# Performance work log

Hardware: AMD Instinct MI355X
Metric: run time of the kernel (lower is better)

## Reference

```python
import jax, jax.numpy as jnp
import numpy as np
import math

H, W = 64, 64
WS = 8            # window_size
KS = 8            # kernel_size (depthwise conv stride=kernel)
D = 512           # d_model
CF = 128          # flow_dModel
IC = D + CF       # 640
HEAD = 8
GH, GW = H // WS, W // WS
G = GH * GW       # windows
EPS = 1e-5


def layernorm(x, g, b):
    m = jnp.mean(x, axis=-1, keepdims=True)
    v = jnp.mean((x - m) ** 2, axis=-1, keepdims=True)
    return (x - m) * jax.lax.rsqrt(v + EPS) * g + b


def depthwise_conv(x_nchw, w, b):
    # w: [C, 1, KS, KS], stride=KS, VALID, groups=C
    y = jax.lax.conv_general_dilated(
        x_nchw, w, window_strides=(KS, KS), padding='VALID',
        feature_group_count=x_nchw.shape[1],
        dimension_numbers=('NCHW', 'OIHW', 'NCHW'))
    return y + b[None, :, None, None]


def setup_inputs() -> dict:
    key = jax.random.key(0)
    ks = jax.random.split(key, 24)
    bt = 8
    s = 0.02
    inp = {
        'x': jax.random.normal(ks[0], (bt, H * W, D), jnp.float32),
        'f': jax.random.normal(ks[1], (bt, H * W, CF), jnp.float32),
        't': 2,
        'Wq': jax.random.normal(ks[2], (IC, D), jnp.float32) * s,
        'bq': jnp.zeros((D,), jnp.float32),
        'Wk': jax.random.normal(ks[3], (IC, D), jnp.float32) * s,
        'bk': jnp.zeros((D,), jnp.float32),
        'Wv': jax.random.normal(ks[4], (D, D), jnp.float32) * s,
        'bv': jnp.zeros((D,), jnp.float32),
        'Wo': jax.random.normal(ks[5], (D, D), jnp.float32) * s,
        'bo': jnp.zeros((D,), jnp.float32),
        'convK_w': jax.random.normal(ks[6], (IC, 1, KS, KS), jnp.float32) * s,
        'convK_b': jnp.zeros((IC,), jnp.float32),
        'convV_w': jax.random.normal(ks[7], (D, 1, KS, KS), jnp.float32) * s,
        'convV_b': jnp.zeros((D,), jnp.float32),
        'qn_g': jnp.ones((IC,), jnp.float32), 'qn_b': jnp.zeros((IC,), jnp.float32),
        'kn_g': jnp.ones((IC,), jnp.float32), 'kn_b': jnp.zeros((IC,), jnp.float32),
        'vn_g': jnp.ones((D,), jnp.float32), 'vn_b': jnp.zeros((D,), jnp.float32),
        'rw_W': jax.random.normal(ks[8], (IC, CF), jnp.float32) * s,
        'rw_b': jnp.zeros((CF,), jnp.float32),
    }
    return inp


def reference(x, f, t, Wq, bq, Wk, bk, Wv, bv, Wo, bo,
              convK_w, convK_b, convV_w, convV_b,
              qn_g, qn_b, kn_g, kn_b, vn_g, vn_b, rw_W, rw_b):
    bt, n, c = x.shape
    hd = c // HEAD
    x4 = x.reshape(bt, H, W, c)            # no padding: H, W multiples of WS
    f4 = f.reshape(bt, H, W, CF)

    xf = jnp.concatenate([x4, f4], axis=-1)                 # [bt,H,W,IC]
    flow_w = jax.nn.sigmoid(xf @ rw_W + rw_b)               # [bt,H,W,CF]
    f4 = f4 * flow_w
    qk = jnp.concatenate([x4, f4], axis=-1)                 # [bt,H,W,IC]

    def windows(a):
        cc = a.shape[-1]
        a = a.reshape(bt, GH, WS, GW, WS, cc).transpose(0, 1, 3, 2, 4, 5)
        return a.reshape(bt, G, WS * WS, cc)

    q = windows(qk)                                          # [bt,G,ws2,IC]

    k_glob = depthwise_conv(qk.transpose(0, 3, 1, 2), convK_w, convK_b)
    k_glob = k_glob.transpose(0, 2, 3, 1).reshape(bt, -1, IC)  # [bt,M,IC]
    M = k_glob.shape[1]
    k_glob = jnp.broadcast_to(k_glob[:, None], (bt, G, M, IC))
    k = jnp.concatenate([q, k_glob], axis=2)                 # [bt,G,ws2+M,IC]

    q = layernorm(q, qn_g, qn_b)
    k = layernorm(k, kn_g, kn_b)

    v_glob = depthwise_conv(x4.transpose(0, 3, 1, 2), convV_w, convV_b)
    v_glob = v_glob.transpose(0, 2, 3, 1).reshape(bt, -1, c)
    v_glob = jnp.broadcast_to(v_glob[:, None], (bt, G, M, c))
    xw = windows(x4)
    v = jnp.concatenate([xw, v_glob], axis=2)                # [bt,G,ws2+M,c]
    v = layernorm(v, vn_g, vn_b)

    query = q @ Wq + bq                                      # [bt,G,ws2,c]
    key = k @ Wk + bk
    value = v @ Wv + bv

    Lk = key.shape[2]
    query = query.reshape(bt, G, WS * WS, HEAD, hd).transpose(0, 1, 3, 2, 4)
    key = key.reshape(bt, G, Lk, HEAD, hd).transpose(0, 1, 3, 2, 4)
    value = value.reshape(bt, G, Lk, HEAD, hd).transpose(0, 1, 3, 2, 4)

    scores = jnp.einsum('bghqd,bghkd->bghqk', query, key) / math.sqrt(hd)
    attn = jax.nn.softmax(scores, axis=-1)
    out = jnp.einsum('bghqk,bghkd->bghqd', attn, value)      # [bt,G,H,ws2,hd]

    out = out.transpose(0, 1, 3, 2, 4).reshape(bt, GH, GW, WS, WS, c)
    out = out.transpose(0, 1, 3, 2, 4, 5).reshape(bt, H, W, c).reshape(bt, n, c)
    return out @ Wo + bo
```

## Files before the change

### kernel.cpp

```cpp
#include <hip/hip_runtime.h>
#include <hip/hip_bf16.h>

typedef __hip_bfloat16 bf16;
typedef __attribute__((ext_vector_type(8))) short bf16x8;
typedef __attribute__((ext_vector_type(8))) unsigned short ushort8;
typedef __attribute__((ext_vector_type(4))) float f32x4;

#define BT 8
#define HH 64
#define WW 64
#define NSP (HH*WW)
#define DD 512
#define CF 128
#define IC 640
#define NG 64
#define NM 64
#define TRI 1536
#define EPS 1e-5f

static __device__ __forceinline__ float b2f(bf16 v) { return __bfloat162float(v); }
static __device__ __forceinline__ bf16 f2b(float v) { return __float2bfloat16(v); }
static __device__ __forceinline__ float u2f(unsigned short u) {
    return __uint_as_float((unsigned)u << 16);
}
static __device__ __forceinline__ unsigned short f2u(float v) {
    bf16 b = __float2bfloat16(v);
    return __builtin_bit_cast(unsigned short, b);
}

__global__ void detect_dtype(const void* __restrict__ x, int* __restrict__ flag) {
    __shared__ int cnt;
    if (threadIdx.x == 0) cnt = 0;
    __syncthreads();
    const unsigned* w = (const unsigned*)x;
    int local = 0;
    for (int i = threadIdx.x; i < 4096; i += 256) {
        float v = __uint_as_float(w[i]);
        float a = fabsf(v);
        if (a > 1e-5f && a < 1e4f) local++;
    }
    atomicAdd(&cnt, local);
    __syncthreads();
    if (threadIdx.x == 0) *flag = (cnt > 2048) ? 1 : 0;
}

#define NW 20
struct WTab {
    const void* src[NW];
    int pre[NW + 1];
};

__global__ void convert_weights(WTab t, const int* __restrict__ flag,
                                bf16* __restrict__ dst, int total) {
    int fp32 = *flag;
    for (int idx = blockIdx.x * blockDim.x + threadIdx.x; idx < total;
         idx += gridDim.x * blockDim.x) {
        int seg = 0;
        #pragma unroll
        for (int i = 0; i < NW; ++i) if (idx >= t.pre[i + 1]) seg = i + 1;
        int local = idx - t.pre[seg];
        bf16 v;
        if (fp32) v = f2b(((const float*)t.src[seg])[local]);
        else      v = ((const bf16*)t.src[seg])[local];
        dst[idx] = v;
    }
}

struct TT {
    int srcoff[5], dstoff[5], R[5], C[5], dstride[5], tpre[6];
};
__global__ void transpose_weights(const bf16* __restrict__ wc, bf16* __restrict__ wt, TT t) {
    __shared__ unsigned short tile[32][33];
    int tb = blockIdx.x;
    int seg = 0;
    while (tb >= t.tpre[seg + 1]) seg++;
    int lt = tb - t.tpre[seg];
    int C = t.C[seg];
    int tpr = C / 32;
    int r0 = (lt / tpr) * 32, c0 = (lt % tpr) * 32;
    int ds = t.dstride[seg];
    const unsigned short* src = (const unsigned short*)(wc + t.srcoff[seg]);
    unsigned short* dst = (unsigned short*)(wt + t.dstoff[seg]);
    int tx = threadIdx.x & 31, ty = threadIdx.x >> 5;
    #pragma unroll
    for (int i = 0; i < 4; ++i)
        tile[ty + i * 8][tx] = src[(long long)(r0 + ty + i * 8) * C + c0 + tx];
    __syncthreads();
    #pragma unroll
    for (int i = 0; i < 4; ++i)
        dst[(long long)(c0 + ty + i * 8) * ds + r0 + tx] = tile[tx][ty + i * 8];
}

__global__ void fold_ln_weights(bf16* __restrict__ WT, int stride,
                                const bf16* __restrict__ g,
                                const bf16* __restrict__ b, const bf16* __restrict__ bias,
                                float* __restrict__ colsum, float* __restrict__ bias2,
                                int K, int Kpad) {
    int n = blockIdx.x;
    bf16* wrow = WT + (long long)n * stride;
    float s1 = 0.f, s2 = 0.f;
    for (int k = threadIdx.x; k < K; k += 256) {
        float w = b2f(wrow[k]);
        float gk = b2f(g[k]);
        wrow[k] = f2b(w * gk);
        s1 += w * gk;
        s2 += w * b2f(b[k]);
    }
    for (int k = K + threadIdx.x; k < Kpad; k += 256) wrow[k] = f2b(0.f);
    __shared__ float r1[256], r2[256];
    r1[threadIdx.x] = s1; r2[threadIdx.x] = s2;
    __syncthreads();
    for (int off = 128; off > 0; off >>= 1) {
        if (threadIdx.x < off) {
            r1[threadIdx.x] += r1[threadIdx.x + off];
            r2[threadIdx.x] += r2[threadIdx.x + off];
        }
        __syncthreads();
    }
    if (threadIdx.x == 0) {
        colsum[n] = r1[0];
        bias2[n]  = b2f(bias[n]) + r2[0];
    }
}

__global__ void assemble_qk_v(const void* __restrict__ xv, const void* __restrict__ fv,
                              const int* __restrict__ flag, bf16* __restrict__ qk,
                              int rows, long long xoff, long long foff) {
    int fp32 = *flag;
    long long total = (long long)rows * 80;
    for (long long i = (long long)blockIdx.x * blockDim.x + threadIdx.x; i < total;
         i += (long long)gridDim.x * blockDim.x) {
        int row = (int)(i / 80);
        int g = (int)(i % 80);
        ushort8 o;
        if (g < 64) {
            long long s = xoff + (long long)row * DD + g * 8;
            if (fp32) {
                const float* xp = (const float*)xv + s;
                #pragma unroll
                for (int e = 0; e < 8; ++e) o[e] = f2u(xp[e]);
            } else {
                o = *(const ushort8*)((const unsigned short*)xv + s);
            }
        } else {
            long long s = foff + (long long)row * CF + (g - 64) * 8;
            if (fp32) {
                const float* fp = (const float*)fv + s;
                #pragma unroll
                for (int e = 0; e < 8; ++e) o[e] = f2u(fp[e]);
            } else {
                o = *(const ushort8*)((const unsigned short*)fv + s);
            }
        }
        *(ushort8*)((unsigned short*)qk + (long long)row * IC + g * 8) = o;
    }
}

__global__ void dwconv_kernel(const bf16* __restrict__ src, int ldr, int C, int ldout,
                              int ldpad,
                              const bf16* __restrict__ w, const bf16* __restrict__ bias,
                              bf16* __restrict__ dst) {
    int bm = blockIdx.x;
    int b = bm >> 6;
    int m = bm & 63;
    int my = m >> 3, mx = m & 7;
    const bf16* sb = src + (long long)b * NSP * ldr;
    for (int c = threadIdx.x; c < C; c += blockDim.x) {
        float acc = b2f(bias[c]);
        #pragma unroll
        for (int ky = 0; ky < 8; ++ky) {
            #pragma unroll
            for (int kx = 0; kx < 8; ++kx) {
                int pos = (my * 8 + ky) * WW + mx * 8 + kx;
                acc += b2f(sb[(long long)pos * ldr + c]) * b2f(w[c * 64 + ky * 8 + kx]);
            }
        }
        dst[(long long)bm * ldout + c] = f2b(acc);
    }
    for (int c = C + threadIdx.x; c < ldpad; c += blockDim.x)
        dst[(long long)bm * ldout + c] = f2b(0.f);
}

__global__ void stats_fused(const bf16* __restrict__ qk, float* __restrict__ stats_full,
                            float* __restrict__ stats_x, int rows) {
    int gt = blockIdx.x * blockDim.x + threadIdx.x;
    int wid = gt >> 6;
    int lane = gt & 63;
    if (wid >= rows) return;
    const unsigned short* p = (const unsigned short*)qk + (long long)wid * IC;
    ushort8 v = *(const ushort8*)(p + lane * 8);
    float s1 = 0.f, ss1 = 0.f, s2 = 0.f, ss2 = 0.f;
    #pragma unroll
    for (int e = 0; e < 8; ++e) { float f = u2f(v[e]); s1 += f; ss1 += f * f; }
    if (lane < 16) {
        ushort8 v2 = *(const ushort8*)(p + DD + lane * 8);
        #pragma unroll
        for (int e = 0; e < 8; ++e) { float f = u2f(v2[e]); s2 += f; ss2 += f * f; }
    }
    #pragma unroll
    for (int off = 32; off > 0; off >>= 1) {
        s1  += __shfl_down(s1,  off, 64);
        ss1 += __shfl_down(ss1, off, 64);
        s2  += __shfl_down(s2,  off, 64);
        ss2 += __shfl_down(ss2, off, 64);
    }
    if (lane == 0) {
        float m1 = s1 / 512.f;
        float var1 = ss1 / 512.f - m1 * m1;
        stats_x[wid * 2]     = m1;
        stats_x[wid * 2 + 1] = rsqrtf(var1 + EPS);
        float st = s1 + s2, sst = ss1 + ss2;
        float m2 = st / 640.f;
        float var2 = sst / 640.f - m2 * m2;
        stats_full[wid * 2]     = m2;
        stats_full[wid * 2 + 1] = rsqrtf(var2 + EPS);
    }
}

__global__ void stats_kernel(const bf16* __restrict__ X, int lda, float* __restrict__ stats,
                             int rows, int K) {
    int gt = blockIdx.x * blockDim.x + threadIdx.x;
    int wid = gt >> 6;
    int lane = gt & 63;
    if (wid >= rows) return;
    const bf16* p = X + (long long)wid * lda;
    float s = 0.f, ss = 0.f;
    for (int k = lane; k < K; k += 64) {
        float v = b2f(p[k]);
        s += v; ss += v * v;
    }
    #pragma unroll
    for (int off = 32; off > 0; off >>= 1) {
        s  += __shfl_down(s,  off, 64);
        ss += __shfl_down(ss, off, 64);
    }
    if (lane == 0) {
        float m = s / K;
        float var = ss / K - m * m;
        stats[wid * 2]     = m;
        stats[wid * 2 + 1] = rsqrtf(var + EPS);
    }
}

__global__ __launch_bounds__(256)
void gemm_mfma(const bf16* __restrict__ A, int lda,
               const float* __restrict__ statsQK, const float* __restrict__ statsX,
               int nQK,
               const float* __restrict__ colsum, const float* __restrict__ bias2,
               const bf16* __restrict__ Bmat,
               const bf16* __restrict__ bias,
               bf16* __restrict__ C,
               void* __restrict__ Cout, const int* __restrict__ outflag, long long outoff,
               const bf16* __restrict__ A2k, const float* __restrict__ stats2k,
               bf16* __restrict__ C2k,
               const bf16* __restrict__ A2v, const float* __restrict__ stats2v,
               bf16* __restrict__ C2v, int M2,
               int M, int N, int K, int mode) {
    __shared__ unsigned short As[128 * 32];
    __shared__ unsigned short Bs[128 * 32];
    int tid = threadIdx.x;

    int nwgx = gridDim.x;
    int nwg = nwgx * gridDim.y;
    int orig = blockIdx.y * nwgx + blockIdx.x;
    int qq = nwg >> 3, rr = nwg & 7;
    int xcd = orig & 7, idx = orig >> 3;
    int wg = (xcd < rr ? xcd * (qq + 1) : rr * (qq + 1) + (xcd - rr) * qq) + idx;
    int gy = wg / nwgx;
    int gx = wg % nwgx;
    int bn = gx * 128;

    int nby_main = M >> 7;
    const bf16* Ap;
    const float* stp = nullptr;
    bf16* C2 = nullptr;
    int rowbase, mlim, glob, colOff = 0;
    if (gy < nby_main) {
        Ap = A; rowbase = gy * 128; mlim = M; glob = 0;
        if (mode == 2) stp = (bn >= nQK) ? statsX : statsQK;
    } else {
        if (bn < 512) return;
        int isV = bn >= 1024;
        Ap = isV ? A2v : A2k;
        stp = isV ? stats2v : stats2k;
        C2 = isV ? C2v : C2k;
        colOff = isV ? 1024 : 512;
        rowbase = (gy - nby_main) * 128; mlim = M2; glob = 1;
    }

    int wave = tid >> 6, lane = tid & 63;
    int qm = (wave >> 1) * 64;
    int qn = (wave & 1) * 64;
    int lm = lane & 15;
    int kq = (lane >> 4) * 8;
    int sr = lane >> 2;
    int sc = (lane & 3) * 8;

    f32x4 acc[4][4];
    #pragma unroll
    for (int i = 0; i < 4; ++i)
        #pragma unroll
        for (int j = 0; j < 4; ++j)
            acc[i][j] = (f32x4){0.f, 0.f, 0.f, 0.f};

    const unsigned short* Au = (const unsigned short*)Ap;
    const unsigned short* Bu = (const unsigned short*)Bmat;

    for (int k0 = 0; k0 < K; k0 += 32) {
        #pragma unroll
        for (int i = 0; i < 2; ++i) {
            int seg = wave * 2 + i;
            const unsigned short* gp =
                Au + (long long)(rowbase + seg * 16 + sr) * lda + k0 + sc;
            __builtin_amdgcn_global_load_lds(
                (const __attribute__((address_space(1))) void*)gp,
                (__attribute__((address_space(3))) void*)&As[seg * 512], 16, 0, 0);
        }
        #pragma unroll
        for (int i = 0; i < 2; ++i) {
            int seg = wave * 2 + i;
            const unsigned short* gp =
                Bu + (long long)(bn + seg * 16 + sr) * K + k0 + sc;
            __builtin_amdgcn_global_load_lds(
                (const __attribute__((address_space(1))) void*)gp,
                (__attribute__((address_space(3))) void*)&Bs[seg * 512], 16, 0, 0);
        }
        __syncthreads();
        bf16x8 af[4], bfr[4];
        #pragma unroll
        for (int i = 0; i < 4; ++i)
            af[i] = *(const bf16x8*)&As[(qm + i * 16 + lm) * 32 + kq];
        #pragma unroll
        for (int j = 0; j < 4; ++j)
            bfr[j] = *(const bf16x8*)&Bs[(qn + j * 16 + lm) * 32 + kq];
        #pragma unroll
        for (int i = 0; i < 4; ++i)
            #pragma unroll
            for (int j = 0; j < 4; ++j)
                acc[i][j] = __builtin_amdgcn_mfma_f32_16x16x32_bf16(
                    af[i], bfr[j], acc[i][j], 0, 0, 0);
        __syncthreads();
    }

    int rq = (lane >> 4) * 4;
    float cs[4], bb[4];
    #pragma unroll
    for (int j = 0; j < 4; ++j) {
        int col = bn + qn + j * 16 + lm;
        if (mode == 2) { cs[j] = colsum[col]; bb[j] = bias2[col]; }
        else bb[j] = bias ? b2f(bias[col]) : 0.f;
    }
    int ofp = (!glob && outflag) ? *outflag : 0;
    #pragma unroll
    for (int i = 0; i < 4; ++i) {
        #pragma unroll
        for (int r = 0; r < 4; ++r) {
            int row = rowbase + qm + i * 16 + rq + r;
            if (row >= mlim) continue;
            float mean = 0.f, rstd = 0.f;
            if (mode == 2) { mean = stp[row * 2]; rstd = stp[row * 2 + 1]; }
            #pragma unroll
            for (int j = 0; j < 4; ++j) {
                int col = bn + qn + j * 16 + lm;
                float v = acc[i][j][r];
                if (mode == 2) v = rstd * (v - mean * cs[j]) + bb[j];
                else {
                    v += bb[j];
                    if (mode == 1 || mode == 3) v = 1.f / (1.f + __expf(-v));
                }
                if (mode == 3) {
                    unsigned short* qp =
                        (unsigned short*)C + (long long)row * IC + DD + col;
                    *qp = f2u(u2f(*qp) * v);
                    continue;
                }
                if (glob) {
                    C2[(long long)row * 512 + (col - colOff)] = f2b(v);
                } else if (outflag) {
                    long long ci = (long long)row * N + col;
                    if (ofp) ((float*)Cout)[outoff + ci] = v;
                    else     ((bf16*)Cout)[outoff + ci] = f2b(v);
                } else {
                    C[(long long)row * N + col] = f2b(v);
                }
            }
        }
    }
}

#define QS_STRIDE 72
#define PS_STRIDE 136
__global__ __launch_bounds__(256)
void attn_kernel(const bf16* __restrict__ qkv,
                 const bf16* __restrict__ key_glob, const bf16* __restrict__ val_glob,
                 bf16* __restrict__ attout) {
    int h = blockIdx.x & 7;
    int g = (blockIdx.x >> 3) & 63;
    int b = blockIdx.x >> 9;
    int gy = g >> 3, gx = g & 7;

    __shared__ unsigned short smem[64 * PS_STRIDE + 64 * PS_STRIDE];
    unsigned short* Qs = smem;
    unsigned short* Ks = smem + 64 * QS_STRIDE;
    unsigned short* Ps = smem;
    unsigned short* Vs = smem + 64 * PS_STRIDE;

    int tid = threadIdx.x;
    const unsigned short* QKV = (const unsigned short*)qkv;
    const unsigned short* KG = (const unsigned short*)key_glob;
    const unsigned short* VG = (const unsigned short*)val_glob;

    #pragma unroll
    for (int it = 0; it < 2; ++it) {
        int i = tid + it * 256;
        int t = i >> 3, dg = (i & 7) * 8;
        int ty = t >> 3, tx = t & 7;
        long long row = (long long)b * NSP + (gy * 8 + ty) * WW + gx * 8 + tx;
        *(ushort8*)&Qs[t * QS_STRIDE + dg] =
            *(const ushort8*)&QKV[row * TRI + h * 64 + dg];
    }
    #pragma unroll
    for (int it = 0; it < 4; ++it) {
        int i = tid + it * 256;
        int t = i >> 3, dg = (i & 7) * 8;
        ushort8 kv;
        if (t < 64) {
            int ty = t >> 3, tx = t & 7;
            long long row = (long long)b * NSP + (gy * 8 + ty) * WW + gx * 8 + tx;
            kv = *(const ushort8*)&QKV[row * TRI + 512 + h * 64 + dg];
        } else {
            long long srow = (long long)b * NM + (t - 64);
            kv = *(const ushort8*)&KG[srow * DD + h * 64 + dg];
        }
        *(ushort8*)&Ks[t * QS_STRIDE + dg] = kv;
    }
    __syncthreads();

    int wave = tid >> 6, lane = tid & 63;
    int m0 = wave * 16;
    int lm = lane & 15;
    int quad = lane >> 4;

    f32x4 sacc[8];
    #pragma unroll
    for (int j = 0; j < 8; ++j) sacc[j] = (f32x4){0.f, 0.f, 0.f, 0.f};
    #pragma unroll
    for (int ks = 0; ks < 2; ++ks) {
        int kq = quad * 8 + ks * 32;
        bf16x8 af = *(const bf16x8*)&Qs[(m0 + lm) * QS_STRIDE + kq];
        #pragma unroll
        for (int j = 0; j < 8; ++j) {
            bf16x8 bfr = *(const bf16x8*)&Ks[(j * 16 + lm) * QS_STRIDE + kq];
            sacc[j] = __builtin_amdgcn_mfma_f32_16x16x32_bf16(af, bfr, sacc[j], 0, 0, 0);
        }
    }
    float pinv[4];
    #pragma unroll
    for (int r = 0; r < 4; ++r) {
        float mx = -1e30f;
        #pragma unroll
        for (int j = 0; j < 8; ++j) {
            sacc[j][r] *= 0.125f;
            mx = fmaxf(mx, sacc[j][r]);
        }
        mx = fmaxf(mx, __shfl_xor(mx, 1, 64));
        mx = fmaxf(mx, __shfl_xor(mx, 2, 64));
        mx = fmaxf(mx, __shfl_xor(mx, 4, 64));
        mx = fmaxf(mx, __shfl_xor(mx, 8, 64));
        float l = 0.f;
        #pragma unroll
        for (int j = 0; j < 8; ++j) {
            float p = __expf(sacc[j][r] - mx);
            sacc[j][r] = p;
            l += p;
        }
        l += __shfl_xor(l, 1, 64);
        l += __shfl_xor(l, 2, 64);
        l += __shfl_xor(l, 4, 64);
        l += __shfl_xor(l, 8, 64);
        pinv[r] = 1.f / l;
    }
    __syncthreads();

    #pragma unroll
    for (int r = 0; r < 4; ++r) {
        int qrow = m0 + quad * 4 + r;
        #pragma unroll
        for (int j = 0; j < 8; ++j)
            Ps[qrow * PS_STRIDE + j * 16 + lm] = f2u(sacc[j][r] * pinv[r]);
    }
    #pragma unroll
    for (int it = 0; it < 4; ++it) {
        int i = tid + it * 256;
        int t = i & 127, dg = (i >> 7) * 8;
        ushort8 v;
        if (t < 64) {
            int ty = t >> 3, tx = t & 7;
            long long row = (long long)b * NSP + (gy * 8 + ty) * WW + gx * 8 + tx;
            v = *(const ushort8*)&QKV[row * TRI + 1024 + h * 64 + dg];
        } else {
            long long srow = (long long)b * NM + (t - 64);
            v = *(const ushort8*)&VG[srow * DD + h * 64 + dg];
        }
        #pragma unroll
        for (int e = 0; e < 8; ++e) Vs[(dg + e) * PS_STRIDE + t] = v[e];
    }
    __syncthreads();

    f32x4 oacc[4];
    #pragma unroll
    for (int j = 0; j < 4; ++j) oacc[j] = (f32x4){0.f, 0.f, 0.f, 0.f};
    #pragma unroll
    for (int ks = 0; ks < 4; ++ks) {
        int kq = quad * 8 + ks * 32;
        bf16x8 af = *(const bf16x8*)&Ps[(m0 + lm) * PS_STRIDE + kq];
        #pragma unroll
        for (int j = 0; j < 4; ++j) {
            bf16x8 bfr = *(const bf16x8*)&Vs[(j * 16 + lm) * PS_STRIDE + kq];
            oacc[j] = __builtin_amdgcn_mfma_f32_16x16x32_bf16(af, bfr, oacc[j], 0, 0, 0);
        }
    }
    #pragma unroll
    for (int r = 0; r < 4; ++r) {
        int qrow = m0 + quad * 4 + r;
        int ty = qrow >> 3, tx = qrow & 7;
        long long orow = (long long)b * NSP + (gy * 8 + ty) * WW + gx * 8 + tx;
        unsigned short* op = (unsigned short*)attout + orow * DD + h * 64;
        #pragma unroll
        for (int j = 0; j < 4; ++j)
            op[j * 16 + lm] = f2u(oacc[j][r]);
    }
}

static inline size_t alg(size_t b) { return (b + 255) & ~(size_t)255; }

extern "C" void kernel_launch(void* const* d_in, const int* in_sizes, int n_in,
                              void* d_out, int out_size, void* d_ws, size_t ws_size,
                              hipStream_t stream) {
    int s = (n_in > 2 && in_sizes[2] == 1) ? 0 : -1;

    const void* xv = d_in[0];
    const void* fv = d_in[1];
    const void* wsrc[NW];
    for (int i = 0; i < NW; ++i) wsrc[i] = d_in[3 + s + i];
    (void)out_size;

    const int wcnt[NW] = {327680, 512, 327680, 512, 262144, 512, 262144, 512,
                          40960, 640, 32768, 512, 640, 640, 640, 640, 512, 512,
                          81920, 128};
    WTab tab;
    int pre = 0;
    for (int i = 0; i < NW; ++i) {
        tab.src[i] = wsrc[i];
        tab.pre[i] = pre;
        pre += wcnt[i];
    }
    tab.pre[NW] = pre;
    const int wtotal = pre;

    char* ws = (char*)d_ws;
    size_t head = 0;
    int* flag = (int*)(ws + head); head += 256;
    bf16* wc = (bf16*)(ws + head); head += alg((size_t)wtotal * 2);
    const int off_qkvW = 0;
    const int off_WoT  = TRI * IC;
    const int off_rwT  = off_WoT + DD * DD;
    const int wtpre    = off_rwT + CF * IC;
    bf16* wt = (bf16*)(ws + head); head += alg((size_t)wtpre * 2);
    float* foldv = (float*)(ws + head); head += alg(2 * TRI * sizeof(float));
    float* cs_qkv = foldv;
    float* b2_qkv = foldv + TRI;

    const bf16* bq     = wc + tab.pre[1];
    const bf16* bk     = wc + tab.pre[3];
    const bf16* bv     = wc + tab.pre[5];
    const bf16* bo     = wc + tab.pre[7];
    const bf16* convKw = wc + tab.pre[8];
    const bf16* convKb = wc + tab.pre[9];
    const bf16* convVw = wc + tab.pre[10];
    const bf16* convVb = wc + tab.pre[11];
    const bf16* qn_g   = wc + tab.pre[12];
    const bf16* qn_b   = wc + tab.pre[13];
    const bf16* kn_g   = wc + tab.pre[14];
    const bf16* kn_b   = wc + tab.pre[15];
    const bf16* vn_g   = wc + tab.pre[16];
    const bf16* vn_b   = wc + tab.pre[17];
    const bf16* rw_b   = wc + tab.pre[19];
    bf16* qkvW = wt + off_qkvW;
    bf16* WoT  = wt + off_WoT;
    bf16* rwT  = wt + off_rwT;

    size_t avail = ws_size > head ? ws_size - head : 0;
    auto need = [&](int bc) -> size_t {
        size_t rows = (size_t)bc * NSP;
        size_t gm = (size_t)bc * NM, gmp = gm + 64;
        return alg(rows * IC * 2) + alg(rows * TRI * 2)
             + 2 * alg(gmp * IC * 2) + 2 * alg(gm * DD * 2)
             + 2 * alg(rows * 8) + 2 * alg(gmp * 8);
    };
    int nb = BT;
    while (nb > 1 && need(nb) > avail) nb--;

    detect_dtype<<<1, 256, 0, stream>>>(xv, flag);
    convert_weights<<<(wtotal + 255) / 256, 256, 0, stream>>>(tab, flag, wc, wtotal);
    {
        TT tt;
        const int srcsel[5]  = {0, 2, 4, 6, 18};
        const int Rr[5]      = {IC, IC, DD, DD, IC};
        const int Cc[5]      = {DD, DD, DD, DD, CF};
        const int dof[5]     = {0, DD * IC, 2 * DD * IC, off_WoT, off_rwT};
        const int dstr[5]    = {IC, IC, IC, DD, IC};
        int tp = 0;
        for (int i = 0; i < 5; ++i) {
            tt.srcoff[i] = tab.pre[srcsel[i]];
            tt.dstoff[i] = dof[i];
            tt.R[i] = Rr[i];
            tt.C[i] = Cc[i];
            tt.dstride[i] = dstr[i];
            tt.tpre[i] = tp;
            tp += (Rr[i] / 32) * (Cc[i] / 32);
        }
        tt.tpre[5] = tp;
        transpose_weights<<<tp, 256, 0, stream>>>(wc, wt, tt);
    }
    fold_ln_weights<<<DD, 256, 0, stream>>>(qkvW,              IC, qn_g, qn_b, bq,
                                            cs_qkv,       b2_qkv,       IC, IC);
    fold_ln_weights<<<DD, 256, 0, stream>>>(qkvW + DD * IC,    IC, kn_g, kn_b, bk,
                                            cs_qkv + 512, b2_qkv + 512, IC, IC);
    fold_ln_weights<<<DD, 256, 0, stream>>>(qkvW + 2 * DD * IC, IC, vn_g, vn_b, bv,
                                            cs_qkv + 1024, b2_qkv + 1024, DD, IC);

    for (int b0 = 0; b0 < BT; b0 += nb) {
        int bc = BT - b0 < nb ? BT - b0 : nb;
        int rows = bc * NSP;
        int gm = bc * NM;
        int gmp = gm + 64;
        int gyg = (gm + 127) / 128;

        size_t off = head;
        auto alloc = [&](size_t bytes) -> void* {
            void* p = ws + off; off += alg(bytes); return p;
        };
        bf16* qk        = (bf16*)alloc((size_t)rows * IC * 2);
        bf16* qkv       = (bf16*)alloc((size_t)rows * TRI * 2);
        bf16* kg        = (bf16*)alloc((size_t)gmp * IC * 2);
        bf16* vg        = (bf16*)alloc((size_t)gmp * IC * 2);
        bf16* key_glob  = (bf16*)alloc((size_t)gm * DD * 2);
        bf16* val_glob  = (bf16*)alloc((size_t)gm * DD * 2);
        float* stats_qk = (float*)alloc((size_t)rows * 8);
        float* stats_x  = (float*)alloc((size_t)rows * 8);
        float* stats_kg = (float*)alloc((size_t)gmp * 8);
        float* stats_vg = (float*)alloc((size_t)gmp * 8);
        bf16* attout    = qk;

        {
            long long total = (long long)rows * 80;
            int blocks = (int)((total + 255) / 256);
            assemble_qk_v<<<blocks, 256, 0, stream>>>(
                xv, fv, flag, qk, rows,
                (long long)b0 * NSP * DD, (long long)b0 * NSP * CF);
        }
        gemm_mfma<<<dim3(CF / 128, rows / 128), 256, 0, stream>>>(
            qk, IC, nullptr, nullptr, 0, nullptr, nullptr, rwT, rw_b, qk,
            nullptr, nullptr, 0,
            nullptr, nullptr, nullptr, nullptr, nullptr, nullptr, 0,
            rows, CF, IC, 3);
        dwconv_kernel<<<bc * NM, 256, 0, stream>>>(qk, IC, IC, IC, IC, convKw, convKb, kg);
        dwconv_kernel<<<bc * NM, 256, 0, stream>>>(qk, IC, DD, IC, IC, convVw, convVb, vg);
        stats_fused<<<rows / 4, 256, 0, stream>>>(qk, stats_qk, stats_x, rows);
        stats_kernel<<<(gm * 64 + 255) / 256, 256, 0, stream>>>(kg, IC, stats_kg, gm, IC);
        stats_kernel<<<(gm * 64 + 255) / 256, 256, 0, stream>>>(vg, IC, stats_vg, gm, DD);
        gemm_mfma<<<dim3(TRI / 128, rows / 128 + gyg), 256, 0, stream>>>(
            qk, IC, stats_qk, stats_x, 1024, cs_qkv, b2_qkv, qkvW, nullptr, qkv,
            nullptr, nullptr, 0,
            kg, stats_kg, key_glob, vg, stats_vg, val_glob, gm,
            rows, TRI, IC, 2);
        attn_kernel<<<bc * NG * 8, 256, 0, stream>>>(qkv, key_glob, val_glob, attout);
        gemm_mfma<<<dim3(DD / 128, rows / 128), 256, 0, stream>>>(
            attout, DD, nullptr, nullptr, 0, nullptr, nullptr, WoT, bo, nullptr,
            d_out, flag, (long long)b0 * NSP * DD,
            nullptr, nullptr, nullptr, nullptr, nullptr, nullptr, 0,
            rows, DD, DD, 0);
    }
}
```

Before: 514.3 us.

## Double-buffer GEMM LDS tiles and fuse depthwise convs with their LayerNorm stats

The MFMA GEMM main loop now uses two LDS buffers, so the global-to-LDS loads for the next K-tile are issued before computing the current one, overlapping memory with MFMA work. Separately, the two depthwise conv kernels and the two stats kernels are merged into one kernel. It reads the qk input once for both K and V convs and reduces the mean and rstd in-block, removing three launches and a re-read of kg/vg. The GEMM loop assumes an even tile count (K/32), which holds for K=640 and 512, and it doubles LDS use. The mode==1 sigmoid branch is also dropped from the epilogue.

```diff
diff --git a/kernel.cpp b/kernel.cpp
--- a/kernel.cpp
+++ b/kernel.cpp
@@ -156,29 +156,66 @@
     }
 }
 
-__global__ void dwconv_kernel(const bf16* __restrict__ src, int ldr, int C, int ldout,
-                              int ldpad,
-                              const bf16* __restrict__ w, const bf16* __restrict__ bias,
-                              bf16* __restrict__ dst) {
+__global__ void dwconv2_kernel(const bf16* __restrict__ qk,
+                               const bf16* __restrict__ wk, const bf16* __restrict__ bk_,
+                               const bf16* __restrict__ wv, const bf16* __restrict__ bv_,
+                               bf16* __restrict__ kg, bf16* __restrict__ vg,
+                               float* __restrict__ stats_kg, float* __restrict__ stats_vg) {
     int bm = blockIdx.x;
     int b = bm >> 6;
     int m = bm & 63;
     int my = m >> 3, mx = m & 7;
-    const bf16* sb = src + (long long)b * NSP * ldr;
-    for (int c = threadIdx.x; c < C; c += blockDim.x) {
-        float acc = b2f(bias[c]);
+    const bf16* sb = qk + (long long)b * NSP * IC;
+    int tid = threadIdx.x;
+    float sk = 0.f, ssk = 0.f, sv = 0.f, ssv = 0.f;
+    for (int c = tid; c < IC; c += 256) {
+        float acc_k = b2f(bk_[c]);
+        bool doV = (c < DD);
+        float acc_v = doV ? b2f(bv_[c]) : 0.f;
         #pragma unroll
         for (int ky = 0; ky < 8; ++ky) {
             #pragma unroll
             for (int kx = 0; kx < 8; ++kx) {
                 int pos = (my * 8 + ky) * WW + mx * 8 + kx;
-                acc += b2f(sb[(long long)pos * ldr + c]) * b2f(w[c * 64 + ky * 8 + kx]);
+                float v = b2f(sb[(long long)pos * IC + c]);
+                acc_k += v * b2f(wk[c * 64 + ky * 8 + kx]);
+                if (doV) acc_v += v * b2f(wv[c * 64 + ky * 8 + kx]);
             }
         }
-        dst[(long long)bm * ldout + c] = f2b(acc);
-    }
-    for (int c = C + threadIdx.x; c < ldpad; c += blockDim.x)
-        dst[(long long)bm * ldout + c] = f2b(0.f);
+        bf16 rk = f2b(acc_k);
+        kg[(long long)bm * IC + c] = rk;
+        float fk = b2f(rk);
+        sk += fk; ssk += fk * fk;
+        if (doV) {
+            bf16 rv = f2b(acc_v);
+            vg[(long long)bm * IC + c] = rv;
+            float fv2 = b2f(rv);
+            sv += fv2; ssv += fv2 * fv2;
+        }
+    }
+    for (int c = DD + tid; c < IC; c += 256) vg[(long long)bm * IC + c] = f2b(0.f);
+    __shared__ float r[4][256];
+    r[0][tid] = sk; r[1][tid] = ssk; r[2][tid] = sv; r[3][tid] = ssv;
+    __syncthreads();
+    for (int off = 128; off > 0; off >>= 1) {
+        if (tid < off) {
+            r[0][tid] += r[0][tid + off];
+            r[1][tid] += r[1][tid + off];
+            r[2][tid] += r[2][tid + off];
+            r[3][tid] += r[3][tid + off];
+        }
+        __syncthreads();
+    }
+    if (tid == 0) {
+        float mk = r[0][0] / IC;
+        float vk = r[1][0] / IC - mk * mk;
+        stats_kg[bm * 2] = mk;
+        stats_kg[bm * 2 + 1] = rsqrtf(vk + EPS);
+        float mv = r[2][0] / DD;
+        float vv = r[3][0] / DD - mv * mv;
+        stats_vg[bm * 2] = mv;
+        stats_vg[bm * 2 + 1] = rsqrtf(vv + EPS);
+    }
 }
 
 __global__ void stats_fused(const bf16* __restrict__ qk, float* __restrict__ stats_full,
@@ -214,31 +251,6 @@
         float var2 = sst / 640.f - m2 * m2;
         stats_full[wid * 2]     = m2;
         stats_full[wid * 2 + 1] = rsqrtf(var2 + EPS);
-    }
-}
-
-__global__ void stats_kernel(const bf16* __restrict__ X, int lda, float* __restrict__ stats,
-                             int rows, int K) {
-    int gt = blockIdx.x * blockDim.x + threadIdx.x;
-    int wid = gt >> 6;
-    int lane = gt & 63;
-    if (wid >= rows) return;
-    const bf16* p = X + (long long)wid * lda;
-    float s = 0.f, ss = 0.f;
-    for (int k = lane; k < K; k += 64) {
-        float v = b2f(p[k]);
-        s += v; ss += v * v;
-    }
-    #pragma unroll
-    for (int off = 32; off > 0; off >>= 1) {
-        s  += __shfl_down(s,  off, 64);
-        ss += __shfl_down(ss, off, 64);
-    }
-    if (lane == 0) {
-        float m = s / K;
-        float var = ss / K - m * m;
-        stats[wid * 2]     = m;
-        stats[wid * 2 + 1] = rsqrtf(var + EPS);
     }
 }
 
@@ -256,8 +268,8 @@
                const bf16* __restrict__ A2v, const float* __restrict__ stats2v,
                bf16* __restrict__ C2v, int M2,
                int M, int N, int K, int mode) {
-    __shared__ unsigned short As[128 * 32];
-    __shared__ unsigned short Bs[128 * 32];
+    __shared__ unsigned short As[2][128 * 32];
+    __shared__ unsigned short Bs[2][128 * 32];
     int tid = threadIdx.x;
 
     int nwgx = gridDim.x;
@@ -305,40 +317,51 @@
 
     const unsigned short* Au = (const unsigned short*)Ap;
     const unsigned short* Bu = (const unsigned short*)Bmat;
-
-    for (int k0 = 0; k0 < K; k0 += 32) {
-        #pragma unroll
-        for (int i = 0; i < 2; ++i) {
-            int seg = wave * 2 + i;
-            const unsigned short* gp =
-                Au + (long long)(rowbase + seg * 16 + sr) * lda + k0 + sc;
-            __builtin_amdgcn_global_load_lds(
-                (const __attribute__((address_space(1))) void*)gp,
-                (__attribute__((address_space(3))) void*)&As[seg * 512], 16, 0, 0);
-        }
-        #pragma unroll
-        for (int i = 0; i < 2; ++i) {
-            int seg = wave * 2 + i;
-            const unsigned short* gp =
-                Bu + (long long)(bn + seg * 16 + sr) * K + k0 + sc;
-            __builtin_amdgcn_global_load_lds(
-                (const __attribute__((address_space(1))) void*)gp,
-                (__attribute__((address_space(3))) void*)&Bs[seg * 512], 16, 0, 0);
-        }
-        __syncthreads();
+    int segA = wave * 2;
+    const unsigned short* a_src0 = Au + (long long)(rowbase + segA * 16 + sr) * lda + sc;
+    const unsigned short* a_src1 = Au + (long long)(rowbase + (segA + 1) * 16 + sr) * lda + sc;
+    const unsigned short* b_src0 = Bu + (long long)(bn + segA * 16 + sr) * K + sc;
+    const unsigned short* b_src1 = Bu + (long long)(bn + (segA + 1) * 16 + sr) * K + sc;
+
+    auto STAGE = [&](int buf, int k0) {
+        __builtin_amdgcn_global_load_lds(
+            (const __attribute__((address_space(1))) void*)(a_src0 + k0),
+            (__attribute__((address_space(3))) void*)&As[buf][segA * 512], 16, 0, 0);
+        __builtin_amdgcn_global_load_lds(
+            (const __attribute__((address_space(1))) void*)(a_src1 + k0),
+            (__attribute__((address_space(3))) void*)&As[buf][(segA + 1) * 512], 16, 0, 0);
+        __builtin_amdgcn_global_load_lds(
+            (const __attribute__((address_space(1))) void*)(b_src0 + k0),
+            (__attribute__((address_space(3))) void*)&Bs[buf][segA * 512], 16, 0, 0);
+        __builtin_amdgcn_global_load_lds(
+            (const __attribute__((address_space(1))) void*)(b_src1 + k0),
+            (__attribute__((address_space(3))) void*)&Bs[buf][(segA + 1) * 512], 16, 0, 0);
+    };
+    auto COMPUTE = [&](int buf) {
         bf16x8 af[4], bfr[4];
         #pragma unroll
         for (int i = 0; i < 4; ++i)
-            af[i] = *(const bf16x8*)&As[(qm + i * 16 + lm) * 32 + kq];
+            af[i] = *(const bf16x8*)&As[buf][(qm + i * 16 + lm) * 32 + kq];
         #pragma unroll
         for (int j = 0; j < 4; ++j)
-            bfr[j] = *(const bf16x8*)&Bs[(qn + j * 16 + lm) * 32 + kq];
+            bfr[j] = *(const bf16x8*)&Bs[buf][(qn + j * 16 + lm) * 32 + kq];
         #pragma unroll
         for (int i = 0; i < 4; ++i)
             #pragma unroll
             for (int j = 0; j < 4; ++j)
                 acc[i][j] = __builtin_amdgcn_mfma_f32_16x16x32_bf16(
                     af[i], bfr[j], acc[i][j], 0, 0, 0);
+    };
+
+    int nt = K >> 5;
+    STAGE(0, 0);
+    __syncthreads();
+    for (int t = 0; t < nt; t += 2) {
+        STAGE(1, (t + 1) << 5);
+        COMPUTE(0);
+        __syncthreads();
+        if (t + 2 < nt) STAGE(0, (t + 2) << 5);
+        COMPUTE(1);
         __syncthreads();
     }
 
@@ -366,7 +389,7 @@
                 if (mode == 2) v = rstd * (v - mean * cs[j]) + bb[j];
                 else {
                     v += bb[j];
-                    if (mode == 1 || mode == 3) v = 1.f / (1.f + __expf(-v));
+                    if (mode == 3) v = 1.f / (1.f + __expf(-v));
                 }
                 if (mode == 3) {
                     unsigned short* qp =
@@ -634,23 +657,23 @@
         int bc = BT - b0 < nb ? BT - b0 : nb;
         int rows = bc * NSP;
         int gm = bc * NM;
-        int gmp = gm + 64;
         int gyg = (gm + 127) / 128;
 
         size_t off = head;
         auto alloc = [&](size_t bytes) -> void* {
             void* p = ws + off; off += alg(bytes); return p;
         };
+        size_t gmp = (size_t)gm + 64;
         bf16* qk        = (bf16*)alloc((size_t)rows * IC * 2);
         bf16* qkv       = (bf16*)alloc((size_t)rows * TRI * 2);
-        bf16* kg        = (bf16*)alloc((size_t)gmp * IC * 2);
-        bf16* vg        = (bf16*)alloc((size_t)gmp * IC * 2);
+        bf16* kg        = (bf16*)alloc(gmp * IC * 2);
+        bf16* vg        = (bf16*)alloc(gmp * IC * 2);
         bf16* key_glob  = (bf16*)alloc((size_t)gm * DD * 2);
         bf16* val_glob  = (bf16*)alloc((size_t)gm * DD * 2);
         float* stats_qk = (float*)alloc((size_t)rows * 8);
         float* stats_x  = (float*)alloc((size_t)rows * 8);
-        float* stats_kg = (float*)alloc((size_t)gmp * 8);
-        float* stats_vg = (float*)alloc((size_t)gmp * 8);
+        float* stats_kg = (float*)alloc(gmp * 8);
+        float* stats_vg = (float*)alloc(gmp * 8);
         bf16* attout    = qk;
 
         {
@@ -665,11 +688,9 @@
             nullptr, nullptr, 0,
             nullptr, nullptr, nullptr, nullptr, nullptr, nullptr, 0,
             rows, CF, IC, 3);
-        dwconv_kernel<<<bc * NM, 256, 0, stream>>>(qk, IC, IC, IC, IC, convKw, convKb, kg);
-        dwconv_kernel<<<bc * NM, 256, 0, stream>>>(qk, IC, DD, IC, IC, convVw, convVb, vg);
+        dwconv2_kernel<<<bc * NM, 256, 0, stream>>>(
+            qk, convKw, convKb, convVw, convVb, kg, vg, stats_kg, stats_vg);
         stats_fused<<<rows / 4, 256, 0, stream>>>(qk, stats_qk, stats_x, rows);
-        stats_kernel<<<(gm * 64 + 255) / 256, 256, 0, stream>>>(kg, IC, stats_kg, gm, IC);
-        stats_kernel<<<(gm * 64 + 255) / 256, 256, 0, stream>>>(vg, IC, stats_vg, gm, DD);
         gemm_mfma<<<dim3(TRI / 128, rows / 128 + gyg), 256, 0, stream>>>(
             qk, IC, stats_qk, stats_x, 1024, cs_qkv, b2_qkv, qkvW, nullptr, qkv,
             nullptr, nullptr, 0,
```

New measurement: 720.5 us. 1.4x slower.

## Fuse K and V depthwise convs into one vectorized kernel with transposed weights

Applied to the files above, without the earlier changes.

Replaces the two per-channel scalar depthwise-conv launches with a single kernel. Each block handles a 64-channel chunk of one window, reads 8 bf16 values per load, and reduces over kernel positions with shuffles plus a small LDS step. The conv weights are pre-transposed to a position-major layout so weight loads coalesce, and each input read is shared between the K and V accumulations. The mode-1 sigmoid branch is also dropped from the GEMM epilogue; that only matters if mode 1 is ever used.

```diff
diff --git a/kernel.cpp b/kernel.cpp
--- a/kernel.cpp
+++ b/kernel.cpp
@@ -66,8 +66,9 @@
     }
 }
 
+#define NSEG 7
 struct TT {
-    int srcoff[5], dstoff[5], R[5], C[5], dstride[5], tpre[6];
+    int srcoff[NSEG], dstoff[NSEG], R[NSEG], C[NSEG], dstride[NSEG], tpre[NSEG + 1];
 };
 __global__ void transpose_weights(const bf16* __restrict__ wc, bf16* __restrict__ wt, TT t) {
     __shared__ unsigned short tile[32][33];
@@ -156,29 +157,72 @@
     }
 }
 
-__global__ void dwconv_kernel(const bf16* __restrict__ src, int ldr, int C, int ldout,
-                              int ldpad,
-                              const bf16* __restrict__ w, const bf16* __restrict__ bias,
-                              bf16* __restrict__ dst) {
-    int bm = blockIdx.x;
-    int b = bm >> 6;
-    int m = bm & 63;
+__global__ __launch_bounds__(256)
+void dwconv_fast(const bf16* __restrict__ qk,
+                 const bf16* __restrict__ wkT, const bf16* __restrict__ bk_,
+                 const bf16* __restrict__ wvT, const bf16* __restrict__ bv_,
+                 bf16* __restrict__ kg, bf16* __restrict__ vg) {
+    int bid = blockIdx.x;
+    int chunk = bid % 10;
+    int bm = bid / 10;
+    int b = bm >> 6, m = bm & 63;
     int my = m >> 3, mx = m & 7;
-    const bf16* sb = src + (long long)b * NSP * ldr;
-    for (int c = threadIdx.x; c < C; c += blockDim.x) {
-        float acc = b2f(bias[c]);
-        #pragma unroll
-        for (int ky = 0; ky < 8; ++ky) {
+    int tid = threadIdx.x;
+    int c8 = tid & 7;
+    int pg = tid >> 3;
+    int cbase = chunk * 64 + c8 * 8;
+    const unsigned short* sb = (const unsigned short*)qk + (long long)b * NSP * IC;
+    const unsigned short* wku = (const unsigned short*)wkT;
+    const unsigned short* wvu = (const unsigned short*)wvT;
+    bool doV = chunk < 8;
+    float ak[8] = {0,0,0,0,0,0,0,0}, av[8] = {0,0,0,0,0,0,0,0};
+    #pragma unroll
+    for (int pp = 0; pp < 2; ++pp) {
+        int p = pg + pp * 32;
+        int ky = p >> 3, kx = p & 7;
+        int pos = (my * 8 + ky) * WW + mx * 8 + kx;
+        ushort8 q = *(const ushort8*)&sb[(long long)pos * IC + cbase];
+        ushort8 wk8 = *(const ushort8*)&wku[p * IC + cbase];
+        #pragma unroll
+        for (int e = 0; e < 8; ++e) ak[e] += u2f(q[e]) * u2f(wk8[e]);
+        if (doV) {
+            ushort8 wv8 = *(const ushort8*)&wvu[p * DD + cbase];
             #pragma unroll
-            for (int kx = 0; kx < 8; ++kx) {
-                int pos = (my * 8 + ky) * WW + mx * 8 + kx;
-                acc += b2f(sb[(long long)pos * ldr + c]) * b2f(w[c * 64 + ky * 8 + kx]);
-            }
-        }
-        dst[(long long)bm * ldout + c] = f2b(acc);
-    }
-    for (int c = C + threadIdx.x; c < ldpad; c += blockDim.x)
-        dst[(long long)bm * ldout + c] = f2b(0.f);
+            for (int e = 0; e < 8; ++e) av[e] += u2f(q[e]) * u2f(wv8[e]);
+        }
+    }
+    #pragma unroll
+    for (int off = 8; off <= 32; off <<= 1) {
+        #pragma unroll
+        for (int e = 0; e < 8; ++e) {
+            ak[e] += __shfl_xor(ak[e], off, 64);
+            av[e] += __shfl_xor(av[e], off, 64);
+        }
+    }
+    __shared__ float lds[2][4][8][8];
+    int wave = tid >> 6, lane = tid & 63;
+    if (lane < 8) {
+        #pragma unroll
+        for (int e = 0; e < 8; ++e) {
+            lds[0][wave][lane][e] = ak[e];
+            lds[1][wave][lane][e] = av[e];
+        }
+    }
+    __syncthreads();
+    if (tid < 64) {
+        int cc8 = tid >> 3, e = tid & 7;
+        int c = chunk * 64 + cc8 * 8 + e;
+        float k4 = lds[0][0][cc8][e] + lds[0][1][cc8][e]
+                 + lds[0][2][cc8][e] + lds[0][3][cc8][e];
+        kg[(long long)bm * IC + c] = f2b(k4 + b2f(bk_[c]));
+        if (doV) {
+            float v4 = lds[1][0][cc8][e] + lds[1][1][cc8][e]
+                     + lds[1][2][cc8][e] + lds[1][3][cc8][e];
+            vg[(long long)bm * IC + c] = f2b(v4 + b2f(bv_[c]));
+        } else {
+            vg[(long long)bm * IC + c] = f2b(0.f);
+        }
+    }
 }
 
 __global__ void stats_fused(const bf16* __restrict__ qk, float* __restrict__ stats_full,
@@ -366,7 +410,7 @@
                 if (mode == 2) v = rstd * (v - mean * cs[j]) + bb[j];
                 else {
                     v += bb[j];
-                    if (mode == 1 || mode == 3) v = 1.f / (1.f + __expf(-v));
+                    if (mode == 3) v = 1.f / (1.f + __expf(-v));
                 }
                 if (mode == 3) {
                     unsigned short* qp =
@@ -565,7 +609,9 @@
     const int off_qkvW = 0;
     const int off_WoT  = TRI * IC;
     const int off_rwT  = off_WoT + DD * DD;
-    const int wtpre    = off_rwT + CF * IC;
+    const int off_wkT  = off_rwT + CF * IC;
+    const int off_wvT  = off_wkT + 64 * IC;
+    const int wtpre    = off_wvT + 64 * DD;
     bf16* wt = (bf16*)(ws + head); head += alg((size_t)wtpre * 2);
     float* foldv = (float*)(ws + head); head += alg(2 * TRI * sizeof(float));
     float* cs_qkv = foldv;
@@ -575,9 +621,7 @@
     const bf16* bk     = wc + tab.pre[3];
     const bf16* bv     = wc + tab.pre[5];
     const bf16* bo     = wc + tab.pre[7];
-    const bf16* convKw = wc + tab.pre[8];
     const bf16* convKb = wc + tab.pre[9];
-    const bf16* convVw = wc + tab.pre[10];
     const bf16* convVb = wc + tab.pre[11];
     const bf16* qn_g   = wc + tab.pre[12];
     const bf16* qn_b   = wc + tab.pre[13];
@@ -589,6 +633,8 @@
     bf16* qkvW = wt + off_qkvW;
     bf16* WoT  = wt + off_WoT;
     bf16* rwT  = wt + off_rwT;
+    bf16* wkT  = wt + off_wkT;
+    bf16* wvT  = wt + off_wvT;
 
     size_t avail = ws_size > head ? ws_size - head : 0;
     auto need = [&](int bc) -> size_t {
@@ -605,13 +651,14 @@
     convert_weights<<<(wtotal + 255) / 256, 256, 0, stream>>>(tab, flag, wc, wtotal);
     {
         TT tt;
-        const int srcsel[5]  = {0, 2, 4, 6, 18};
-        const int Rr[5]      = {IC, IC, DD, DD, IC};
-        const int Cc[5]      = {DD, DD, DD, DD, CF};
-        const int dof[5]     = {0, DD * IC, 2 * DD * IC, off_WoT, off_rwT};
-        const int dstr[5]    = {IC, IC, IC, DD, IC};
+        const int srcsel[NSEG] = {0, 2, 4, 6, 18, 8, 10};
+        const int Rr[NSEG]     = {IC, IC, DD, DD, IC, IC, DD};
+        const int Cc[NSEG]     = {DD, DD, DD, DD, CF, 64, 64};
+        const int dof[NSEG]    = {0, DD * IC, 2 * DD * IC, off_WoT, off_rwT,
+                                  off_wkT, off_wvT};
+        const int dstr[NSEG]   = {IC, IC, IC, DD, IC, IC, DD};
         int tp = 0;
-        for (int i = 0; i < 5; ++i) {
+        for (int i = 0; i < NSEG; ++i) {
             tt.srcoff[i] = tab.pre[srcsel[i]];
             tt.dstoff[i] = dof[i];
             tt.R[i] = Rr[i];
@@ -620,7 +667,7 @@
             tt.tpre[i] = tp;
             tp += (Rr[i] / 32) * (Cc[i] / 32);
         }
-        tt.tpre[5] = tp;
+        tt.tpre[NSEG] = tp;
         transpose_weights<<<tp, 256, 0, stream>>>(wc, wt, tt);
     }
     fold_ln_weights<<<DD, 256, 0, stream>>>(qkvW,              IC, qn_g, qn_b, bq,
@@ -634,23 +681,23 @@
         int bc = BT - b0 < nb ? BT - b0 : nb;
         int rows = bc * NSP;
         int gm = bc * NM;
-        int gmp = gm + 64;
         int gyg = (gm + 127) / 128;
 
         size_t off = head;
         auto alloc = [&](size_t bytes) -> void* {
             void* p = ws + off; off += alg(bytes); return p;
         };
+        size_t gmp = (size_t)gm + 64;
         bf16* qk        = (bf16*)alloc((size_t)rows * IC * 2);
         bf16* qkv       = (bf16*)alloc((size_t)rows * TRI * 2);
-        bf16* kg        = (bf16*)alloc((size_t)gmp * IC * 2);
-        bf16* vg        = (bf16*)alloc((size_t)gmp * IC * 2);
+        bf16* kg        = (bf16*)alloc(gmp * IC * 2);
+        bf16* vg        = (bf16*)alloc(gmp * IC * 2);
         bf16* key_glob  = (bf16*)alloc((size_t)gm * DD * 2);
         bf16* val_glob  = (bf16*)alloc((size_t)gm * DD * 2);
         float* stats_qk = (float*)alloc((size_t)rows * 8);
         float* stats_x  = (float*)alloc((size_t)rows * 8);
-        float* stats_kg = (float*)alloc((size_t)gmp * 8);
-        float* stats_vg = (float*)alloc((size_t)gmp * 8);
+        float* stats_kg = (float*)alloc(gmp * 8);
+        float* stats_vg = (float*)alloc(gmp * 8);
         bf16* attout    = qk;
 
         {
@@ -665,8 +712,8 @@
             nullptr, nullptr, 0,
             nullptr, nullptr, nullptr, nullptr, nullptr, nullptr, 0,
             rows, CF, IC, 3);
-        dwconv_kernel<<<bc * NM, 256, 0, stream>>>(qk, IC, IC, IC, IC, convKw, convKb, kg);
-        dwconv_kernel<<<bc * NM, 256, 0, stream>>>(qk, IC, DD, IC, IC, convVw, convVb, vg);
+        dwconv_fast<<<bc * NM * 10, 256, 0, stream>>>(
+            qk, wkT, convKb, wvT, convVb, kg, vg);
         stats_fused<<<rows / 4, 256, 0, stream>>>(qk, stats_qk, stats_x, rows);
         stats_kernel<<<(gm * 64 + 255) / 256, 256, 0, stream>>>(kg, IC, stats_kg, gm, IC);
         stats_kernel<<<(gm * 64 + 255) / 256, 256, 0, stream>>>(vg, IC, stats_vg, gm, DD);
```

Measured after the change: 500.4 us. 1.03x faster.
